# Optimization experiments

Measured on AMD Instinct MI355X. Metric: run time of the kernel, lower is better.

The kernel has to match this reference:

```python
import jax, jax.numpy as jnp
import numpy as np
import math

B, L, D, H = 4, 2048, 1024, 16
DH = D // H


def setup_inputs() -> dict:
    key = jax.random.key(0)
    ks = jax.random.split(key, 12)
    s = 0.02
    q = jax.random.normal(ks[0], (B, L, D), jnp.float32)
    k = jax.random.normal(ks[1], (B, L, D), jnp.float32)
    v = jax.random.normal(ks[2], (B, L, D), jnp.float32)
    # realistic padding: each sequence has a valid prefix of length in [L//2, L]
    lengths = jax.random.randint(ks[3], (B,), L // 2, L + 1)
    attention_mask = jnp.arange(L)[None, :] < lengths[:, None]  # [B, L] bool
    Wq = jax.random.normal(ks[4], (D, D), jnp.float32) * s
    bq = jnp.zeros((D,), jnp.float32)
    Wk = jax.random.normal(ks[5], (D, D), jnp.float32) * s
    bk = jnp.zeros((D,), jnp.float32)
    Wv = jax.random.normal(ks[6], (D, D), jnp.float32) * s
    bv = jnp.zeros((D,), jnp.float32)
    Wc = jax.random.normal(ks[7], (D, D), jnp.float32) * s
    bc = jnp.zeros((D,), jnp.float32)
    return {"q": q, "k": k, "v": v, "attention_mask": attention_mask,
            "Wq": Wq, "bq": bq, "Wk": Wk, "bk": bk,
            "Wv": Wv, "bv": bv, "Wc": Wc, "bc": bc}


def reference(q, k, v, attention_mask, Wq, bq, Wk, bk, Wv, bv, Wc, bc):
    b, l, d = q.shape
    # projections -> [B, H, L, DH]
    wq = (q @ Wq.T + bq).reshape(b, l, H, DH).transpose(0, 2, 1, 3)
    wk = (k @ Wk.T + bk).reshape(b, l, H, DH).transpose(0, 2, 1, 3)
    wv = (v @ Wv.T + bv).reshape(b, l, H, DH).transpose(0, 2, 1, 3)
    scores = jnp.einsum('bhqd,bhkd->bhqk', wq, wk) / math.sqrt(DH)  # [B,H,L,L]
    # fused causal + padding mask (additive, finfo.min like the torch code)
    pad2d = attention_mask[:, :, None] & attention_mask[:, None, :]  # [B,L,L]
    causal = jnp.tril(jnp.ones((l, l), dtype=bool))
    mask = pad2d[:, None, :, :] & causal[None, None, :, :]  # [B,1,L,L] -> broadcast over heads
    min_val = jnp.finfo(scores.dtype).min
    scores = scores + jnp.where(mask, jnp.float32(0.0), min_val).astype(scores.dtype)
    att = jax.nn.softmax(scores, axis=-1)
    out = jnp.einsum('bhqk,bhkd->bhqd', att, wv)  # [B,H,L,DH]
    out = out.transpose(0, 2, 1, 3).reshape(b, l, H * DH)
    return out @ Wc.T + bc
```

## Files before the change

kernel.cpp:

```cpp
#include <hip/hip_runtime.h>
#include <stdint.h>

typedef __bf16 bf16x8 __attribute__((ext_vector_type(8)));
typedef float f32x4 __attribute__((ext_vector_type(4)));
typedef unsigned short ushort8 __attribute__((ext_vector_type(8)));
typedef unsigned short ushort4v __attribute__((ext_vector_type(4)));

constexpr int CB = 4;
constexpr int CL = 2048;
constexpr int CD = 1024;
constexpr int CH = 16;
constexpr int CDH = 64;
constexpr int CM = CB * CL;

__device__ __forceinline__ unsigned short f2bf(float f) {
  union { float f; unsigned u; } x; x.f = f;
  unsigned r = x.u + 0x7fffu + ((x.u >> 16) & 1u);
  return (unsigned short)(r >> 16);
}
__device__ __forceinline__ float bf2f(unsigned short b) {
  union { unsigned u; float f; } x; x.u = ((unsigned)b) << 16;
  return x.f;
}

__device__ __forceinline__ void gld_lds16(const void* g, void* l) {
  __builtin_amdgcn_global_load_lds((const __attribute__((address_space(1))) void*)g,
                                   (__attribute__((address_space(3))) void*)l, 16, 0, 0);
}

#define MFMA16(a, b, c) __builtin_amdgcn_mfma_f32_16x16x32_bf16((a), (b), (c), 0, 0, 0)


__global__ __launch_bounds__(256) void cvt3_kernel(const float* __restrict__ q,
                                                   const float* __restrict__ k,
                                                   const float* __restrict__ v,
                                                   unsigned short* __restrict__ oq,
                                                   unsigned short* __restrict__ ok,
                                                   unsigned short* __restrict__ ov) {
  const int which = blockIdx.x >> 12;
  const int i = (blockIdx.x & 4095) * 256 + threadIdx.x;
  const float* s = which == 0 ? q : which == 1 ? k : v;
  unsigned short* d = which == 0 ? oq : which == 1 ? ok : ov;
  const float4* sp = (const float4*)s;
  float4 a = sp[2 * i], b = sp[2 * i + 1];
  ushort8 o;
  o[0] = f2bf(a.x); o[1] = f2bf(a.y); o[2] = f2bf(a.z); o[3] = f2bf(a.w);
  o[4] = f2bf(b.x); o[5] = f2bf(b.y); o[6] = f2bf(b.z); o[7] = f2bf(b.w);
  ((ushort8*)d)[i] = o;
}

__global__ __launch_bounds__(256) void cvtw_kernel(const float* w0, const float* w1,
                                                   const float* w2, const float* w3,
                                                   unsigned short* o0, unsigned short* o1,
                                                   unsigned short* o2, unsigned short* o3) {
  const int which = blockIdx.x >> 9;
  const int i = (blockIdx.x & 511) * 256 + threadIdx.x;
  const float* s = which == 0 ? w0 : which == 1 ? w1 : which == 2 ? w2 : w3;
  unsigned short* d = which == 0 ? o0 : which == 1 ? o1 : which == 2 ? o2 : o3;
  const float4* sp = (const float4*)s;
  float4 a = sp[2 * i], b = sp[2 * i + 1];
  ushort8 o;
  o[0] = f2bf(a.x); o[1] = f2bf(a.y); o[2] = f2bf(a.z); o[3] = f2bf(a.w);
  o[4] = f2bf(b.x); o[5] = f2bf(b.y); o[6] = f2bf(b.z); o[7] = f2bf(b.w);
  ((ushort8*)d)[i] = o;
}


__global__ __launch_bounds__(256) void lens_kernel(const int* __restrict__ mask,
                                                   int* __restrict__ lens) {
  __shared__ int part[4];
  const int b = blockIdx.x;
  int cnt = 0;
  for (int i = threadIdx.x; i < CL; i += 256) cnt += (mask[b * CL + i] != 0) ? 1 : 0;
#pragma unroll
  for (int off = 32; off; off >>= 1) cnt += __shfl_down(cnt, off);
  if ((threadIdx.x & 63) == 0) part[threadIdx.x >> 6] = cnt;
  __syncthreads();
  if (threadIdx.x == 0) lens[b] = part[0] + part[1] + part[2] + part[3];
}


#define GEMM_WAIT2(kt, nkt)                                             \
  {                                                                     \
    if ((kt) + 1 < (nkt))                                               \
      asm volatile("s_waitcnt vmcnt(2)" ::: "memory");                  \
    else                                                                \
      asm volatile("s_waitcnt vmcnt(0)" ::: "memory");                  \
    __builtin_amdgcn_s_barrier();                                       \
    asm volatile("" ::: "memory");                                      \
  }


__global__ __launch_bounds__(512) void gemm_qkv(const unsigned short* __restrict__ Xq,
                                                const unsigned short* __restrict__ Xk,
                                                const unsigned short* __restrict__ Xv,
                                                const unsigned short* __restrict__ Wb,
                                                const float* __restrict__ bq,
                                                const float* __restrict__ bk,
                                                const float* __restrict__ bv,
                                                unsigned short* __restrict__ Qp,
                                                unsigned short* __restrict__ Kp,
                                                unsigned short* __restrict__ Vt,
                                                float qscale) {
  __shared__ unsigned short Asm[3][128 * 32];
  __shared__ unsigned short Bsm[3][128 * 32];
  const int tid = threadIdx.x;
  const int w = tid >> 6, ln = tid & 63, lr = ln & 15, lq = ln >> 4;
  const int nbx = 24;
  const int cpx = (int)gridDim.x >> 3;
  const int bid = ((int)blockIdx.x & 7) * cpx + ((int)blockIdx.x >> 3);
  const int bm = (bid / nbx) << 7;
  const int bnG = (bid % nbx) << 7;
  const int which = bnG >> 10, bn = bnG & 1023;
  const unsigned short* A = which == 0 ? Xq : which == 1 ? Xk : Xv;
  const unsigned short* Bw = Wb + ((size_t)which << 20);
  const float* bias = which == 0 ? bq : which == 1 ? bk : bv;
  const float alpha = which == 0 ? qscale : 1.0f;
  const int wr = (w >> 1) << 5, wc = (w & 1) << 6;

  f32x4 acc[2][4] = {};
  const int arow = tid >> 2, akc = (tid & 3) << 3;

  auto stage = [&](int buf, int k0) {
    gld_lds16(A + (size_t)(bm + arow) * CD + k0 + akc, (void*)(Asm[buf] + w * 512));
    gld_lds16(Bw + (size_t)(bn + arow) * CD + k0 + akc, (void*)(Bsm[buf] + w * 512));
  };

  stage(0, 0);
  stage(1, 32);

  const int nkt = CD >> 5;
  int cur = 0;
  for (int kt = 0; kt < nkt; ++kt) {
    GEMM_WAIT2(kt, nkt);
    if (kt + 2 < nkt) {
      int nb = cur + 2;
      if (nb >= 3) nb -= 3;
      stage(nb, (kt + 2) << 5);
    }
    bf16x8 af[2], bfr[4];
#pragma unroll
    for (int f = 0; f < 2; ++f)
      af[f] = *(const bf16x8*)(Asm[cur] + ((wr + f * 16 + lr) * 32 + lq * 8));
#pragma unroll
    for (int f = 0; f < 4; ++f)
      bfr[f] = *(const bf16x8*)(Bsm[cur] + ((wc + f * 16 + lr) * 32 + lq * 8));
#pragma unroll
    for (int fm = 0; fm < 2; ++fm)
#pragma unroll
      for (int fn = 0; fn < 4; ++fn)
        acc[fm][fn] = MFMA16(af[fm], bfr[fn], acc[fm][fn]);
    if (++cur == 3) cur = 0;
  }

#pragma unroll
  for (int fm = 0; fm < 2; ++fm) {
    const int row0 = bm + wr + fm * 16 + lq * 4;
#pragma unroll
    for (int fn = 0; fn < 4; ++fn) {
      const int col = bn + wc + fn * 16 + lr;
      const float bb = bias[col];
      if (which == 2) {
        const int b = row0 >> 11, lrow = row0 & (CL - 1);
        const int hh = col >> 6, dh = col & 63;
        ushort4v pk;
#pragma unroll
        for (int j = 0; j < 4; ++j) pk[j] = f2bf(acc[fm][fn][j] + bb);
        *(ushort4v*)(Vt + (((size_t)((b * CH + hh) * CDH + dh)) << 11) + lrow) = pk;
      } else {
        unsigned short* outp = which == 0 ? Qp : Kp;
#pragma unroll
        for (int j = 0; j < 4; ++j)
          outp[(size_t)(row0 + j) * CD + col] = f2bf((acc[fm][fn][j] + bb) * alpha);
      }
    }
  }
}


__global__ __launch_bounds__(512) void gemm_out(const unsigned short* __restrict__ A,
                                                const unsigned short* __restrict__ Bw,
                                                const float* __restrict__ bias,
                                                float* __restrict__ Cout) {
  __shared__ unsigned short Asm[3][128 * 32];
  __shared__ unsigned short Bsm[3][128 * 32];
  const int tid = threadIdx.x;
  const int w = tid >> 6, ln = tid & 63, lr = ln & 15, lq = ln >> 4;
  const int nbx = CD >> 7;
  const int cpx = (int)gridDim.x >> 3;
  const int bid = ((int)blockIdx.x & 7) * cpx + ((int)blockIdx.x >> 3);
  const int bm = (bid / nbx) << 7;
  const int bn = (bid % nbx) << 7;
  const int wr = (w >> 1) << 5, wc = (w & 1) << 6;

  f32x4 acc[2][4] = {};
  const int arow = tid >> 2, akc = (tid & 3) << 3;

  auto stage = [&](int buf, int k0) {
    gld_lds16(A + (size_t)(bm + arow) * CD + k0 + akc, (void*)(Asm[buf] + w * 512));
    gld_lds16(Bw + (size_t)(bn + arow) * CD + k0 + akc, (void*)(Bsm[buf] + w * 512));
  };

  stage(0, 0);
  stage(1, 32);

  const int nkt = CD >> 5;
  int cur = 0;
  for (int kt = 0; kt < nkt; ++kt) {
    GEMM_WAIT2(kt, nkt);
    if (kt + 2 < nkt) {
      int nb = cur + 2;
      if (nb >= 3) nb -= 3;
      stage(nb, (kt + 2) << 5);
    }
    bf16x8 af[2], bfr[4];
#pragma unroll
    for (int f = 0; f < 2; ++f)
      af[f] = *(const bf16x8*)(Asm[cur] + ((wr + f * 16 + lr) * 32 + lq * 8));
#pragma unroll
    for (int f = 0; f < 4; ++f)
      bfr[f] = *(const bf16x8*)(Bsm[cur] + ((wc + f * 16 + lr) * 32 + lq * 8));
#pragma unroll
    for (int fm = 0; fm < 2; ++fm)
#pragma unroll
      for (int fn = 0; fn < 4; ++fn)
        acc[fm][fn] = MFMA16(af[fm], bfr[fn], acc[fm][fn]);
    if (++cur == 3) cur = 0;
  }

#pragma unroll
  for (int fm = 0; fm < 2; ++fm) {
    const int row0 = bm + wr + fm * 16 + lq * 4;
#pragma unroll
    for (int fn = 0; fn < 4; ++fn) {
      const int col = bn + wc + fn * 16 + lr;
      const float bb = bias[col];
#pragma unroll
      for (int j = 0; j < 4; ++j)
        Cout[(size_t)(row0 + j) * CD + col] = acc[fm][fn][j] + bb;
    }
  }
}


__global__ __launch_bounds__(256) void meanv_kernel(const unsigned short* __restrict__ Vt,
                                                    float* __restrict__ meanv) {
  const int row = blockIdx.x * 4 + (threadIdx.x >> 6);
  const int ln = threadIdx.x & 63;
  const ushort8* p = (const ushort8*)(Vt + (size_t)row * CL);
  float s = 0.f;
#pragma unroll
  for (int it = 0; it < 4; ++it) {
    ushort8 v = p[it * 64 + ln];
#pragma unroll
    for (int j = 0; j < 8; ++j) s += bf2f(v[j]);
  }
#pragma unroll
  for (int off = 32; off; off >>= 1) s += __shfl_down(s, off);
  if (ln == 0) meanv[row] = s * (1.f / (float)CL);
}


#define LOADK(kt, dst)                                                              \
  {                                                                                 \
    const int kb_ = (kt) << 6;                                                      \
    for (int cf_ = 0; cf_ < 4; ++cf_)                                               \
      for (int hf_ = 0; hf_ < 2; ++hf_)                                             \
        dst[cf_][hf_] = *(const bf16x8*)(Kbase + (size_t)(kb_ + cf_ * 16 + lr) * CD + \
                                         hf_ * 32 + lq * 8);                        \
  }

#define VLOAD_FB(kt, dst)                                                           \
  {                                                                                 \
    const int kb_ = (kt) << 6;                                                      \
    for (int df_ = 0; df_ < 4; ++df_)                                               \
      for (int hf_ = 0; hf_ < 2; ++hf_)                                             \
        dst[df_][hf_] = *(const bf16x8*)(Vbase + (((size_t)(df_ * 16 + lr)) << 11) +  \
                                         kb_ + hf_ * 32 + lq * 8);                  \
  }

#define TILE_FB(kt, KF, KN)                                                         \
  {                                                                                 \
    const bool dm_ = (kt) == kdiag;                                                 \
    const int kb_ = (kt) << 6;                                                      \
    f32x4 s_[2][4];                                                                 \
    for (int rs_ = 0; rs_ < 2; ++rs_)                                               \
      for (int cf_ = 0; cf_ < 4; ++cf_) {                                           \
        f32x4 z_ = {};                                                              \
        z_ = MFMA16(qa[rs_][0], KF[cf_][0], z_);                                    \
        z_ = MFMA16(qa[rs_][1], KF[cf_][1], z_);                                    \
        s_[rs_][cf_] = z_;                                                          \
      }                                                                             \
    VLOAD_FB(kt, vb);                                                               \
    if ((kt) < kdiag) LOADK((kt) + 1, KN);                                          \
    __builtin_amdgcn_sched_barrier(0);                                              \
    for (int rs_ = 0; rs_ < 2; ++rs_)                                               \
      for (int cf_ = 0; cf_ < 4; ++cf_)                                             \
        for (int j_ = 0; j_ < 4; ++j_) {                                            \
          float p_ = __builtin_amdgcn_exp2f(s_[rs_][cf_][j_]);                      \
          if (dm_) {                                                                \
            const int key_ = kb_ + cf_ * 16 + lr;                                   \
            const int row_ = rowbase + rs_ * 16 + lq * 4 + j_;                      \
            p_ = (key_ > row_) ? 0.f : p_;                                          \
          }                                                                         \
          lsum[rs_][j_] += p_;                                                      \
          Ps[rs_ * 16 + lq * 4 + j_][cf_ * 16 + lr] =                               \
              (unsigned short)(__builtin_bit_cast(unsigned int, p_) >> 16);         \
        }                                                                           \
    bf16x8 pa_[2][2];                                                               \
    for (int rs_ = 0; rs_ < 2; ++rs_)                                               \
      for (int hf_ = 0; hf_ < 2; ++hf_)                                             \
        pa_[rs_][hf_] = *(const bf16x8*)(&Ps[rs_ * 16 + lr][hf_ * 32 + lq * 8]);    \
    for (int df_ = 0; df_ < 4; ++df_) {                                             \
      o[0][df_] = MFMA16(pa_[0][0], vb[df_][0], o[0][df_]);                         \
      o[0][df_] = MFMA16(pa_[0][1], vb[df_][1], o[0][df_]);                         \
      o[1][df_] = MFMA16(pa_[1][0], vb[df_][0], o[1][df_]);                         \
      o[1][df_] = MFMA16(pa_[1][1], vb[df_][1], o[1][df_]);                         \
    }                                                                               \
  }

__global__ __launch_bounds__(64, 2) void attn_fb(const unsigned short* __restrict__ Qp,
                                                 const unsigned short* __restrict__ Kp,
                                                 const unsigned short* __restrict__ Vt,
                                                 const int* __restrict__ lens,
                                                 unsigned short* __restrict__ attno) {
  __shared__ unsigned short Ps[32][72];
  const int i = blockIdx.x;
  const int xcd = i & 7, bh8 = (i >> 3) & 7, slot = i >> 6;
  const int qt = 15 - (slot >> 2), wv = slot & 3;
  const int bh = bh8 * 8 + xcd;
  const int b = bh >> 4, h = bh & 15;
  const int rowbase = (qt << 7) + (wv << 5);
  const int len = lens[b];
  if (rowbase >= len) return;

  const int tid = threadIdx.x, lr = tid & 15, lq = tid >> 4;

  const unsigned short* Kbase = Kp + (size_t)(b * CL) * CD + h * 64;
  const unsigned short* Vbase = Vt + ((size_t)(bh * 64) << 11);
  const unsigned short* Qbase = Qp + (size_t)(b * CL + rowbase) * CD + h * 64;

  bf16x8 qa[2][2];
#pragma unroll
  for (int rs = 0; rs < 2; ++rs)
#pragma unroll
    for (int hf = 0; hf < 2; ++hf)
      qa[rs][hf] = *(const bf16x8*)(Qbase + (size_t)(rs * 16 + lr) * CD + hf * 32 + lq * 8);

  f32x4 o[2][4] = {};
  float lsum[2][4] = {};
  const int kdiag = rowbase >> 6;

  bf16x8 kfA[4][2], kfB[4][2], vb[4][2];
  LOADK(0, kfA);

  int kt = 0;
  while (true) {
    TILE_FB(kt, kfA, kfB);
    if (kt == kdiag) break;
    ++kt;
    TILE_FB(kt, kfB, kfA);
    if (kt == kdiag) break;
    ++kt;
  }

  float inv[2][4];
#pragma unroll
  for (int rs = 0; rs < 2; ++rs)
#pragma unroll
    for (int j = 0; j < 4; ++j) {
      float t = lsum[rs][j];
      t += __shfl_xor(t, 1);
      t += __shfl_xor(t, 2);
      t += __shfl_xor(t, 4);
      t += __shfl_xor(t, 8);
      inv[rs][j] = __builtin_amdgcn_rcpf(t);
    }

#pragma unroll
  for (int rs = 0; rs < 2; ++rs)
#pragma unroll
    for (int df = 0; df < 4; ++df)
#pragma unroll
      for (int j = 0; j < 4; ++j)
        attno[(size_t)(b * CL + rowbase + rs * 16 + lq * 4 + j) * CD + h * 64 + df * 16 +
              lr] = f2bf(o[rs][df][j] * inv[rs][j]);
}


__global__ __launch_bounds__(256) void padfix_kernel(const int* __restrict__ lens,
                                                     const float* __restrict__ meanv,
                                                     unsigned short* __restrict__ attno) {
  const int q = blockIdx.x & (CL - 1);
  const int b = blockIdx.x >> 11;
  if (q < lens[b]) return;
#pragma unroll
  for (int i = 0; i < 4; ++i) {
    const int col = threadIdx.x + i * 256;
    attno[(size_t)(b * CL + q) * CD + col] = f2bf(meanv[b * CD + col]);
  }
}


extern "C" void kernel_launch(void* const* d_in, const int* in_sizes, int n_in,
                              void* d_out, int out_size, void* d_ws, size_t ws_size,
                              hipStream_t stream) {
  const float* q  = (const float*)d_in[0];
  const float* k  = (const float*)d_in[1];
  const float* v  = (const float*)d_in[2];
  const int*   am = (const int*)d_in[3];
  const float* Wq = (const float*)d_in[4];
  const float* bq = (const float*)d_in[5];
  const float* Wk = (const float*)d_in[6];
  const float* bk = (const float*)d_in[7];
  const float* Wv = (const float*)d_in[8];
  const float* bv = (const float*)d_in[9];
  const float* Wc = (const float*)d_in[10];
  const float* bc = (const float*)d_in[11];
  float* out = (float*)d_out;

  unsigned short* Wqb = (unsigned short*)d_ws;
  unsigned short* Wkb = Wqb + (1 << 20);
  unsigned short* Wvb = Wkb + (1 << 20);
  unsigned short* Wcb = Wvb + (1 << 20);
  unsigned short* Xq  = Wcb + (1 << 20);
  unsigned short* Xk  = Xq + (size_t)CM * CD;
  unsigned short* Xv  = Xk + (size_t)CM * CD;
  unsigned short* Qp  = Xv + (size_t)CM * CD;
  unsigned short* Kp  = Qp + (size_t)CM * CD;
  unsigned short* Vt  = Kp + (size_t)CM * CD;
  float* meanv = (float*)(Vt + (size_t)CM * CD);
  int* lens = (int*)(meanv + CB * CD);
  unsigned short* X = Xq;

  cvtw_kernel<<<2048, 256, 0, stream>>>(Wq, Wk, Wv, Wc, Wqb, Wkb, Wvb, Wcb);
  lens_kernel<<<CB, 256, 0, stream>>>(am, lens);
  cvt3_kernel<<<12288, 256, 0, stream>>>(q, k, v, Xq, Xk, Xv);

  const float QSCALE = 0.125f * 1.44269504f;

  gemm_qkv<<<1536, 512, 0, stream>>>(Xq, Xk, Xv, Wqb, bq, bk, bv, Qp, Kp, Vt, QSCALE);

  meanv_kernel<<<1024, 256, 0, stream>>>(Vt, meanv);

  attn_fb<<<4096, 64, 0, stream>>>(Qp, Kp, Vt, lens, X);
  padfix_kernel<<<CB * CL, 256, 0, stream>>>(lens, meanv, X);

  gemm_out<<<512, 512, 0, stream>>>(X, Wcb, bc, out);
}
```

Measured before the change: 226.6 us.

## Add 64-row-per-wave attention kernel and merge conversion kernels into one launch

```diff
diff --git a/kernel.cpp b/kernel.cpp
--- a/kernel.cpp
+++ b/kernel.cpp
@@ -31,32 +31,36 @@
 #define MFMA16(a, b, c) __builtin_amdgcn_mfma_f32_16x16x32_bf16((a), (b), (c), 0, 0, 0)
 
 
-__global__ __launch_bounds__(256) void cvt3_kernel(const float* __restrict__ q,
-                                                   const float* __restrict__ k,
-                                                   const float* __restrict__ v,
-                                                   unsigned short* __restrict__ oq,
-                                                   unsigned short* __restrict__ ok,
-                                                   unsigned short* __restrict__ ov) {
-  const int which = blockIdx.x >> 12;
-  const int i = (blockIdx.x & 4095) * 256 + threadIdx.x;
-  const float* s = which == 0 ? q : which == 1 ? k : v;
-  unsigned short* d = which == 0 ? oq : which == 1 ? ok : ov;
-  const float4* sp = (const float4*)s;
-  float4 a = sp[2 * i], b = sp[2 * i + 1];
-  ushort8 o;
-  o[0] = f2bf(a.x); o[1] = f2bf(a.y); o[2] = f2bf(a.z); o[3] = f2bf(a.w);
-  o[4] = f2bf(b.x); o[5] = f2bf(b.y); o[6] = f2bf(b.z); o[7] = f2bf(b.w);
-  ((ushort8*)d)[i] = o;
-}
-
-__global__ __launch_bounds__(256) void cvtw_kernel(const float* w0, const float* w1,
-                                                   const float* w2, const float* w3,
-                                                   unsigned short* o0, unsigned short* o1,
-                                                   unsigned short* o2, unsigned short* o3) {
-  const int which = blockIdx.x >> 9;
-  const int i = (blockIdx.x & 511) * 256 + threadIdx.x;
-  const float* s = which == 0 ? w0 : which == 1 ? w1 : which == 2 ? w2 : w3;
-  unsigned short* d = which == 0 ? o0 : which == 1 ? o1 : which == 2 ? o2 : o3;
+__global__ __launch_bounds__(256) void cvt_all(const float* __restrict__ q,
+                                               const float* __restrict__ k,
+                                               const float* __restrict__ v,
+                                               const float* __restrict__ Wq,
+                                               const float* __restrict__ Wk,
+                                               const float* __restrict__ Wv,
+                                               const float* __restrict__ Wc,
+                                               unsigned short* __restrict__ oq,
+                                               unsigned short* __restrict__ ok,
+                                               unsigned short* __restrict__ ov,
+                                               unsigned short* __restrict__ oWq,
+                                               unsigned short* __restrict__ oWk,
+                                               unsigned short* __restrict__ oWv,
+                                               unsigned short* __restrict__ oWc) {
+  int bi = blockIdx.x;
+  const float* s;
+  unsigned short* d;
+  int i;
+  if (bi < 2048) {
+    const int w = bi >> 9;
+    i = (bi & 511) * 256 + threadIdx.x;
+    s = w == 0 ? Wq : w == 1 ? Wk : w == 2 ? Wv : Wc;
+    d = w == 0 ? oWq : w == 1 ? oWk : w == 2 ? oWv : oWc;
+  } else {
+    bi -= 2048;
+    const int w = bi >> 12;
+    i = (bi & 4095) * 256 + threadIdx.x;
+    s = w == 0 ? q : w == 1 ? k : v;
+    d = w == 0 ? oq : w == 1 ? ok : ov;
+  }
   const float4* sp = (const float4*)s;
   float4 a = sp[2 * i], b = sp[2 * i + 1];
   ushort8 o;
@@ -278,6 +282,116 @@
         dst[df_][hf_] = *(const bf16x8*)(Vbase + (((size_t)(df_ * 16 + lr)) << 11) +  \
                                          kb_ + hf_ * 32 + lq * 8);                  \
   }
+
+
+__global__ __launch_bounds__(64, 2) void attn_w64(const unsigned short* __restrict__ Qp,
+                                                  const unsigned short* __restrict__ Kp,
+                                                  const unsigned short* __restrict__ Vt,
+                                                  const int* __restrict__ lens,
+                                                  unsigned short* __restrict__ attno) {
+  __shared__ unsigned short Ps[64][72];
+  const int i = blockIdx.x;
+  const int xcd = i & 7, bh8 = (i >> 3) & 7, slot = i >> 6;
+  const int qc = 31 - slot;
+  const int bh = bh8 * 8 + xcd;
+  const int b = bh >> 4, h = bh & 15;
+  const int rowbase = qc << 6;
+  const int len = lens[b];
+  if (rowbase >= len) return;
+
+  const int tid = threadIdx.x, lr = tid & 15, lq = tid >> 4;
+
+  const unsigned short* Kbase = Kp + (size_t)(b * CL) * CD + h * 64;
+  const unsigned short* Vbase = Vt + ((size_t)(bh * 64) << 11);
+  const unsigned short* Qbase = Qp + (size_t)(b * CL + rowbase) * CD + h * 64;
+
+  bf16x8 qa[4][2];
+#pragma unroll
+  for (int rs = 0; rs < 4; ++rs)
+#pragma unroll
+    for (int hf = 0; hf < 2; ++hf)
+      qa[rs][hf] = *(const bf16x8*)(Qbase + (size_t)(rs * 16 + lr) * CD + hf * 32 + lq * 8);
+
+  f32x4 o[4][4] = {};
+  float lsum[4][4] = {};
+  const int kdiag = qc;
+
+  bf16x8 kf[4][2], vb[4][2];
+
+  for (int kt = 0; kt <= kdiag; ++kt) {
+    const bool dm = (kt == kdiag);
+    const int kb = kt << 6;
+    LOADK(kt, kf);
+    VLOAD_FB(kt, vb);
+    __builtin_amdgcn_sched_barrier(0);
+
+#pragma unroll
+    for (int rs = 0; rs < 4; ++rs) {
+      f32x4 s_[4];
+#pragma unroll
+      for (int cf = 0; cf < 4; ++cf) {
+        f32x4 z = {};
+        z = MFMA16(qa[rs][0], kf[cf][0], z);
+        z = MFMA16(qa[rs][1], kf[cf][1], z);
+        s_[cf] = z;
+      }
+#pragma unroll
+      for (int cf = 0; cf < 4; ++cf) {
+#pragma unroll
+        for (int j = 0; j < 4; ++j) {
+          float p = __builtin_amdgcn_exp2f(s_[cf][j]);
+          if (dm) {
+            const int key = kb + cf * 16 + lr;
+            const int row = rowbase + rs * 16 + lq * 4 + j;
+            p = (key > row) ? 0.f : p;
+          }
+          lsum[rs][j] += p;
+          Ps[rs * 16 + lq * 4 + j][cf * 16 + lr] =
+              (unsigned short)(__builtin_bit_cast(unsigned int, p) >> 16);
+        }
+      }
+    }
+
+    bf16x8 pa[4][2];
+#pragma unroll
+    for (int rs = 0; rs < 4; ++rs)
+#pragma unroll
+      for (int hf = 0; hf < 2; ++hf)
+        pa[rs][hf] = *(const bf16x8*)(&Ps[rs * 16 + lr][hf * 32 + lq * 8]);
+
+#pragma unroll
+    for (int df = 0; df < 4; ++df) {
+#pragma unroll
+      for (int rs = 0; rs < 4; ++rs) {
+        o[rs][df] = MFMA16(pa[rs][0], vb[df][0], o[rs][df]);
+        o[rs][df] = MFMA16(pa[rs][1], vb[df][1], o[rs][df]);
+      }
+    }
+  }
+
+  float inv[4][4];
+#pragma unroll
+  for (int rs = 0; rs < 4; ++rs)
+#pragma unroll
+    for (int j = 0; j < 4; ++j) {
+      float t = lsum[rs][j];
+      t += __shfl_xor(t, 1);
+      t += __shfl_xor(t, 2);
+      t += __shfl_xor(t, 4);
+      t += __shfl_xor(t, 8);
+      inv[rs][j] = __builtin_amdgcn_rcpf(t);
+    }
+
+#pragma unroll
+  for (int rs = 0; rs < 4; ++rs)
+#pragma unroll
+    for (int df = 0; df < 4; ++df)
+#pragma unroll
+      for (int j = 0; j < 4; ++j)
+        attno[(size_t)(b * CL + rowbase + rs * 16 + lq * 4 + j) * CD + h * 64 + df * 16 +
+              lr] = f2bf(o[rs][df][j] * inv[rs][j]);
+}
+
 
 #define TILE_FB(kt, KF, KN)                                                         \
   {                                                                                 \
@@ -433,9 +547,9 @@
   int* lens = (int*)(meanv + CB * CD);
   unsigned short* X = Xq;
 
-  cvtw_kernel<<<2048, 256, 0, stream>>>(Wq, Wk, Wv, Wc, Wqb, Wkb, Wvb, Wcb);
   lens_kernel<<<CB, 256, 0, stream>>>(am, lens);
-  cvt3_kernel<<<12288, 256, 0, stream>>>(q, k, v, Xq, Xk, Xv);
+  cvt_all<<<14336, 256, 0, stream>>>(q, k, v, Wq, Wk, Wv, Wc, Xq, Xk, Xv,
+                                     Wqb, Wkb, Wvb, Wcb);
 
   const float QSCALE = 0.125f * 1.44269504f;
 
@@ -443,7 +557,15 @@
 
   meanv_kernel<<<1024, 256, 0, stream>>>(Vt, meanv);
 
-  attn_fb<<<4096, 64, 0, stream>>>(Qp, Kp, Vt, lens, X);
+  hipFuncAttributes fa{};
+  bool w64_ok = false;
+  if (hipFuncGetAttributes(&fa, (const void*)attn_w64) == hipSuccess)
+    w64_ok = (fa.localSizeBytes == 0);
+  if (w64_ok)
+    attn_w64<<<2048, 64, 0, stream>>>(Qp, Kp, Vt, lens, X);
+  else
+    attn_fb<<<4096, 64, 0, stream>>>(Qp, Kp, Vt, lens, X);
+
   padfix_kernel<<<CB * CL, 256, 0, stream>>>(lens, meanv, X);
 
   gemm_out<<<512, 512, 0, stream>>>(X, Wcb, bc, out);
```

New measurement: 226.8 us. No clear change (+0.1%).
